# Kernel tuning notes

Hardware: AMD Instinct MI355X
Metric: run time of the kernel (lower is better)

Reference implementation:

```python
import jax, jax.numpy as jnp
import numpy as np

OMEGA = 30.0

def _conv1x1(x, W, b):
    # x: [B, Cin, D, H, W]; W: [Cout, Cin]; b: [Cout]
    return jnp.einsum('oi,bidhw->bodhw', W, x) + b[None, :, None, None, None]

def setup_inputs() -> dict:
    key = jax.random.key(0)
    ks = jax.random.split(key, 12)
    B, D, H, Wd = 1, 8, 128, 128
    C = 256
    shp = (B, 3, D, H, Wd)
    std = np.sqrt(6.0 / C) / OMEGA
    return {
        'z': jax.random.normal(ks[0], shp, jnp.float32),
        'n': jax.random.normal(ks[1], shp, jnp.float32),
        'ad': jax.random.normal(ks[2], shp, jnp.float32),
        's': jax.random.normal(ks[3], shp, jnp.float32),
        'pixel_coords': jax.random.uniform(ks[4], shp, jnp.float32),
        'view_direction': jax.random.normal(ks[5], shp, jnp.float32),
        'W1': jax.random.normal(ks[6], (C, 12), jnp.float32) * std,
        'b1': jax.random.normal(ks[7], (C,), jnp.float32) * std,
        'W2': jax.random.normal(ks[8], (C, C), jnp.float32) * std,
        'b2': jax.random.normal(ks[9], (C,), jnp.float32) * std,
        'W4': jax.random.normal(ks[10], (3, C), jnp.float32) * 1e-4,
        'b4': jax.random.normal(ks[11], (3,), jnp.float32) * 1e-4,
    }

def reference(z, n, ad, s, pixel_coords, view_direction, W1, b1, W2, b2, W4, b4):
    # concat along channel dim: [B, 12, D, H, W]
    x = jnp.concatenate((s, n, pixel_coords, view_direction), axis=1)
    h = jnp.sin(OMEGA * _conv1x1(x, W1, b1))
    h = jnp.sin(OMEGA * _conv1x1(h, W2, b2))
    s_out = 0.5 * jnp.sin(OMEGA * _conv1x1(h, W4, b4))
    # lighting_predict_mode == 'total'
    return z + s_out
```

## Files before the change

### kernel.cpp

```cpp
#include <hip/hip_runtime.h>
#include <hip/hip_bf16.h>

#define NPIX (8*128*128)
#define CH   256

typedef __attribute__((ext_vector_type(8))) short bf16x8;
typedef __attribute__((ext_vector_type(4))) float f32x4;

__device__ inline unsigned int pkbf(float a, float b) {
    union { __hip_bfloat162 h; unsigned int u; } c;
    c.h = __float22bfloat162_rn(float2{a, b});
    return c.u;
}
__device__ inline unsigned short f2bf(float f) {
    unsigned int u = __float_as_uint(f);
    return (unsigned short)((u + 0x7FFFu + ((u >> 16) & 1u)) >> 16);
}

__global__ __launch_bounds__(256) void conv_weights(
    const float* __restrict__ W1, const float* __restrict__ W2,
    const float* __restrict__ W4,
    unsigned short* __restrict__ W2b, unsigned short* __restrict__ W1b,
    unsigned short* __restrict__ W4b)
{
    if (blockIdx.x < 256) {
        const int i = blockIdx.x * 256 + threadIdx.x;
        W2b[i] = f2bf(W2[i]);
    } else {
        const int t = threadIdx.x;
        #pragma unroll
        for (int j = 0; j < 16; ++j)
            W1b[t*16 + j] = (j < 12) ? f2bf(W1[t*12 + j]) : (unsigned short)0;
        #pragma unroll
        for (int r = 0; r < 16; ++r)
            W4b[r*CH + t] = (r < 3) ? f2bf(W4[r*CH + t]) : (unsigned short)0;
    }
}

template<bool PRE>
__global__ __launch_bounds__(256, 3) void rendernet_fused2(
    const float* __restrict__ z,
    const float* __restrict__ nrm,
    const float* __restrict__ sph,
    const float* __restrict__ pc,
    const float* __restrict__ vd,
    const float* __restrict__ W1,
    const float* __restrict__ b1,
    const float* __restrict__ W2f,
    const unsigned short* __restrict__ W2b,
    const unsigned short* __restrict__ W1b,
    const float* __restrict__ b2,
    const float* __restrict__ W4f,
    const unsigned short* __restrict__ W4b,
    const float* __restrict__ b4,
    float* __restrict__ out)
{
    __shared__ __align__(16) char smem[64*512 + 64*80];
    char* xb = smem + 64*512;

    const int tid     = threadIdx.x;
    const int lane    = tid & 63;
    const int wave    = tid >> 6;
    const int lm      = lane & 15;
    const int lg      = lane >> 4;
    const int n0      = wave * 64;
    const int pixbase = blockIdx.x * 64;

    if constexpr (PRE) {
        {
            const int gp = pixbase + lane;
            union { unsigned int w[4]; bf16x8 v; } t;
            t.w[0] = t.w[1] = t.w[2] = t.w[3] = 0u;
            if (wave == 0) {
                t.w[0] = pkbf(sph[0*NPIX+gp], sph[1*NPIX+gp]);
                t.w[1] = pkbf(sph[2*NPIX+gp], nrm[0*NPIX+gp]);
                t.w[2] = pkbf(nrm[1*NPIX+gp], nrm[2*NPIX+gp]);
                t.w[3] = pkbf(pc [0*NPIX+gp], pc [1*NPIX+gp]);
            } else if (wave == 1) {
                t.w[0] = pkbf(pc[2*NPIX+gp], vd[0*NPIX+gp]);
                t.w[1] = pkbf(vd[1*NPIX+gp], vd[2*NPIX+gp]);
            }
            *(bf16x8*)(xb + lane*80 + wave*16) = t.v;
        }
        __syncthreads();

        f32x4 a1c[4][4];
        #pragma unroll
        for (int i = 0; i < 4; ++i)
            #pragma unroll
            for (int j = 0; j < 4; ++j) a1c[i][j] = (f32x4){0.f,0.f,0.f,0.f};

        bf16x8 w1frag[4];
        #pragma unroll
        for (int nf = 0; nf < 4; ++nf) {
            const int row = n0 + nf*16 + lm;
            bf16x8 t = *(const bf16x8*)(W1b + row*16 + (lg & 1)*8);
            w1frag[nf] = (lg < 2) ? t : (bf16x8){0,0,0,0,0,0,0,0};
        }
        bf16x8 ax[4];
        #pragma unroll
        for (int mf = 0; mf < 4; ++mf)
            ax[mf] = *(const bf16x8*)(xb + (mf*16 + lm)*80 + lg*16);

        #pragma unroll
        for (int nf = 0; nf < 4; ++nf)
            #pragma unroll
            for (int mf = 0; mf < 4; ++mf)
                a1c[mf][nf] = __builtin_amdgcn_mfma_f32_16x16x32_bf16(
                                  ax[mf], w1frag[nf], a1c[mf][nf], 0, 0, 0);

        float b1v[4];
        #pragma unroll
        for (int nf = 0; nf < 4; ++nf) b1v[nf] = b1[n0 + nf*16 + lm];

        #pragma unroll
        for (int mf = 0; mf < 4; ++mf)
            #pragma unroll
            for (int nf = 0; nf < 4; ++nf)
                #pragma unroll
                for (int r = 0; r < 4; ++r) {
                    const int pix = mf*16 + lg*4 + r;
                    const int ch  = n0 + nf*16 + lm;
                    *(unsigned short*)(smem + pix*512 + ((ch*2) ^ ((pix & 31) << 4))) =
                        f2bf(__sinf(30.0f * (a1c[mf][nf][r] + b1v[nf])));
                }
    } else {
        const int gp  = pixbase + lane;
        const int swz = (lane & 31) << 4;
        float xv[12];
        #pragma unroll
        for (int k = 0; k < 3; ++k) xv[k]     = sph[k*NPIX + gp];
        #pragma unroll
        for (int k = 0; k < 3; ++k) xv[3 + k] = nrm[k*NPIX + gp];
        #pragma unroll
        for (int k = 0; k < 3; ++k) xv[6 + k] = pc [k*NPIX + gp];
        #pragma unroll
        for (int k = 0; k < 3; ++k) xv[9 + k] = vd [k*NPIX + gp];
        #pragma unroll
        for (int cc = 0; cc < 64; cc += 8) {
            float hv[8];
            #pragma unroll
            for (int u = 0; u < 8; ++u) {
                const int c = n0 + cc + u;
                float a = b1[c];
                #pragma unroll
                for (int k = 0; k < 12; ++k) a += W1[c*12 + k] * xv[k];
                hv[u] = __sinf(30.0f * a);
            }
            union { unsigned int w[4]; bf16x8 v; } tp;
            #pragma unroll
            for (int u = 0; u < 4; ++u) tp.w[u] = pkbf(hv[2*u], hv[2*u+1]);
            *(bf16x8*)(smem + lane*512 + (((n0 + cc)*2) ^ swz)) = tp.v;
        }
    }
    __syncthreads();

    float b2v[4];
    #pragma unroll
    for (int nf = 0; nf < 4; ++nf) b2v[nf] = b2[n0 + nf*16 + lm];

    f32x4 acc[4][4];
    #pragma unroll
    for (int i = 0; i < 4; ++i)
        #pragma unroll
        for (int j = 0; j < 4; ++j) acc[i][j] = (f32x4){0.f,0.f,0.f,0.f};

    if constexpr (PRE) {
        const unsigned short* bp = W2b + (n0 + lm)*CH + lg*8;
        #pragma unroll
        for (int k0i = 0; k0i < 8; ++k0i) {
            bf16x8 bfr[4];
            #pragma unroll
            for (int nf = 0; nf < 4; ++nf)
                bfr[nf] = *(const bf16x8*)(bp + nf*16*CH + k0i*32);
            bf16x8 afr[4];
            #pragma unroll
            for (int mf = 0; mf < 4; ++mf) {
                const int pr = mf*16 + lm;
                afr[mf] = *(const bf16x8*)(smem + pr*512 +
                              (((k0i*32 + lg*8)*2) ^ ((pr & 31) << 4)));
            }
            #pragma unroll
            for (int nf = 0; nf < 4; ++nf)
                #pragma unroll
                for (int mf = 0; mf < 4; ++mf)
                    acc[mf][nf] = __builtin_amdgcn_mfma_f32_16x16x32_bf16(
                                      afr[mf], bfr[nf], acc[mf][nf], 0, 0, 0);
        }
    } else {
        const float* wp = W2f + (n0 + lm)*CH + lg*8;
        #pragma unroll
        for (int k0i = 0; k0i < 8; ++k0i) {
            bf16x8 afr[4];
            #pragma unroll
            for (int mf = 0; mf < 4; ++mf) {
                const int pr = mf*16 + lm;
                afr[mf] = *(const bf16x8*)(smem + pr*512 +
                              (((k0i*32 + lg*8)*2) ^ ((pr & 31) << 4)));
            }
            #pragma unroll
            for (int nf = 0; nf < 4; ++nf) {
                f32x4 lo = *(const f32x4*)(wp + nf*16*CH + k0i*32);
                f32x4 hi = *(const f32x4*)(wp + nf*16*CH + k0i*32 + 4);
                union { unsigned int w[4]; bf16x8 v; } t;
                t.w[0] = pkbf(lo[0], lo[1]);  t.w[1] = pkbf(lo[2], lo[3]);
                t.w[2] = pkbf(hi[0], hi[1]);  t.w[3] = pkbf(hi[2], hi[3]);
                #pragma unroll
                for (int mf = 0; mf < 4; ++mf)
                    acc[mf][nf] = __builtin_amdgcn_mfma_f32_16x16x32_bf16(
                                      afr[mf], t.v, acc[mf][nf], 0, 0, 0);
            }
        }
    }
    __syncthreads();

    #pragma unroll
    for (int mf = 0; mf < 4; ++mf)
        #pragma unroll
        for (int nf = 0; nf < 4; ++nf)
            #pragma unroll
            for (int r = 0; r < 4; ++r) {
                const int pix = mf*16 + lg*4 + r;
                const int ch  = n0 + nf*16 + lm;
                *(unsigned short*)(smem + pix*512 + ((ch*2) ^ ((pix & 31) << 4))) =
                    f2bf(__sinf(30.0f * (acc[mf][nf][r] + b2v[nf])));
            }
    __syncthreads();

    if (wave == 0) {
        bf16x8 w4r[8];
        if constexpr (PRE) {
            const unsigned short* bp = W4b + lm*CH + lg*8;
            #pragma unroll
            for (int k0i = 0; k0i < 8; ++k0i)
                w4r[k0i] = *(const bf16x8*)(bp + k0i*32);
        } else {
            const int c3 = (lm < 3) ? lm : 2;
            const float* fp = W4f + c3*CH + lg*8;
            #pragma unroll
            for (int k0i = 0; k0i < 8; ++k0i) {
                f32x4 lo = *(const f32x4*)(fp + k0i*32);
                f32x4 hi = *(const f32x4*)(fp + k0i*32 + 4);
                union { unsigned int w[4]; bf16x8 v; } tc;
                tc.w[0] = pkbf(lo[0], lo[1]);  tc.w[1] = pkbf(lo[2], lo[3]);
                tc.w[2] = pkbf(hi[0], hi[1]);  tc.w[3] = pkbf(hi[2], hi[3]);
                w4r[k0i] = tc.v;
            }
        }

        f32x4 d[4];
        #pragma unroll
        for (int i = 0; i < 4; ++i) d[i] = (f32x4){0.f,0.f,0.f,0.f};

        #pragma unroll
        for (int k0i = 0; k0i < 8; ++k0i) {
            bf16x8 afr[4];
            #pragma unroll
            for (int mf = 0; mf < 4; ++mf) {
                const int pr = mf*16 + lm;
                afr[mf] = *(const bf16x8*)(smem + pr*512 +
                              (((k0i*32 + lg*8)*2) ^ ((pr & 31) << 4)));
            }
            #pragma unroll
            for (int mf = 0; mf < 4; ++mf)
                d[mf] = __builtin_amdgcn_mfma_f32_16x16x32_bf16(
                            afr[mf], w4r[k0i], d[mf], 0, 0, 0);
        }

        if (lm < 3) {
            const float b4v = b4[lm];
            #pragma unroll
            for (int mf = 0; mf < 4; ++mf)
                #pragma unroll
                for (int r = 0; r < 4; ++r) {
                    const int pix = mf*16 + lg*4 + r;
                    const int gi  = lm*NPIX + pixbase + pix;
                    out[gi] = z[gi] + 0.5f * __sinf(30.0f * (d[mf][r] + b4v));
                }
        }
    }
}

extern "C" void kernel_launch(void* const* d_in, const int* in_sizes, int n_in,
                              void* d_out, int out_size, void* d_ws, size_t ws_size,
                              hipStream_t stream) {
    const float* z   = (const float*)d_in[0];
    const float* nrm = (const float*)d_in[1];
    const float* s   = (const float*)d_in[3];
    const float* pc  = (const float*)d_in[4];
    const float* vd  = (const float*)d_in[5];
    const float* W1  = (const float*)d_in[6];
    const float* b1  = (const float*)d_in[7];
    const float* W2  = (const float*)d_in[8];
    const float* b2  = (const float*)d_in[9];
    const float* W4  = (const float*)d_in[10];
    const float* b4  = (const float*)d_in[11];
    float* out = (float*)d_out;

    const size_t need = (size_t)(CH*CH + 16*CH + 16*CH) * sizeof(unsigned short);
    if (ws_size >= need) {
        unsigned short* W2b = (unsigned short*)d_ws;
        unsigned short* W1b = W2b + CH*CH;
        unsigned short* W4b = W1b + 16*CH;
        conv_weights<<<dim3(257), dim3(256), 0, stream>>>(W1, W2, W4, W2b, W1b, W4b);
        rendernet_fused2<true><<<dim3(NPIX/64), dim3(256), 0, stream>>>(
            z, nrm, s, pc, vd, W1, b1, W2, W2b, W1b, b2, W4, W4b, b4, out);
    } else {
        rendernet_fused2<false><<<dim3(NPIX/64), dim3(256), 0, stream>>>(
            z, nrm, s, pc, vd, W1, b1, W2, nullptr, nullptr, b2, W4, nullptr, b4, out);
    }
}
```

Before: 143.4 us.

## Split channels across eight waves with permuted K layout and packed stores

Raises the block to 512 threads (8 waves), so each wave covers 32 output channels instead of 64. This halves per-wave accumulator registers and aims for more waves per CU. The K dimension of W2 and W4 is permuted at conversion time so each lane can write two adjacent channels as one packed 32-bit store to LDS instead of scalar 16-bit stores. Biases are folded into the accumulator initialisation. In exchange the weight fragment reuse per wave drops and W2 is read by twice as many waves per block.

```diff
diff --git a/kernel.cpp b/kernel.cpp
--- a/kernel.cpp
+++ b/kernel.cpp
@@ -15,6 +15,9 @@
 __device__ inline unsigned short f2bf(float f) {
     unsigned int u = __float_as_uint(f);
     return (unsigned short)((u + 0x7FFFu + ((u >> 16) & 1u)) >> 16);
+}
+__device__ inline int kperm32(int k) {
+    return (k & ~31) | ((k & 15) << 1) | ((k >> 4) & 1);
 }
 
 __global__ __launch_bounds__(256) void conv_weights(
@@ -24,21 +27,22 @@
     unsigned short* __restrict__ W4b)
 {
     if (blockIdx.x < 256) {
-        const int i = blockIdx.x * 256 + threadIdx.x;
-        W2b[i] = f2bf(W2[i]);
+        const int o = blockIdx.x, k = threadIdx.x;
+        W2b[o*CH + kperm32(k)] = f2bf(W2[o*CH + k]);
     } else {
         const int t = threadIdx.x;
         #pragma unroll
         for (int j = 0; j < 16; ++j)
             W1b[t*16 + j] = (j < 12) ? f2bf(W1[t*12 + j]) : (unsigned short)0;
+        const int kp = kperm32(t);
         #pragma unroll
         for (int r = 0; r < 16; ++r)
-            W4b[r*CH + t] = (r < 3) ? f2bf(W4[r*CH + t]) : (unsigned short)0;
+            W4b[r*CH + kp] = (r < 3) ? f2bf(W4[r*CH + t]) : (unsigned short)0;
     }
 }
 
 template<bool PRE>
-__global__ __launch_bounds__(256, 3) void rendernet_fused2(
+__global__ __launch_bounds__(512, 4) void rendernet3(
     const float* __restrict__ z,
     const float* __restrict__ nrm,
     const float* __restrict__ sph,
@@ -63,39 +67,42 @@
     const int wave    = tid >> 6;
     const int lm      = lane & 15;
     const int lg      = lane >> 4;
-    const int n0      = wave * 64;
+    const int n0      = wave * 32;
     const int pixbase = blockIdx.x * 64;
+
+    f32x4 acc[4][2];
 
     if constexpr (PRE) {
         {
             const int gp = pixbase + lane;
-            union { unsigned int w[4]; bf16x8 v; } t;
-            t.w[0] = t.w[1] = t.w[2] = t.w[3] = 0u;
+            unsigned int w0 = 0u, w1 = 0u;
             if (wave == 0) {
-                t.w[0] = pkbf(sph[0*NPIX+gp], sph[1*NPIX+gp]);
-                t.w[1] = pkbf(sph[2*NPIX+gp], nrm[0*NPIX+gp]);
-                t.w[2] = pkbf(nrm[1*NPIX+gp], nrm[2*NPIX+gp]);
-                t.w[3] = pkbf(pc [0*NPIX+gp], pc [1*NPIX+gp]);
+                w0 = pkbf(sph[0*NPIX+gp], sph[1*NPIX+gp]);
+                w1 = pkbf(sph[2*NPIX+gp], nrm[0*NPIX+gp]);
             } else if (wave == 1) {
-                t.w[0] = pkbf(pc[2*NPIX+gp], vd[0*NPIX+gp]);
-                t.w[1] = pkbf(vd[1*NPIX+gp], vd[2*NPIX+gp]);
-            }
-            *(bf16x8*)(xb + lane*80 + wave*16) = t.v;
+                w0 = pkbf(nrm[1*NPIX+gp], nrm[2*NPIX+gp]);
+                w1 = pkbf(pc [0*NPIX+gp], pc [1*NPIX+gp]);
+            } else if (wave == 2) {
+                w0 = pkbf(pc[2*NPIX+gp], vd[0*NPIX+gp]);
+                w1 = pkbf(vd[1*NPIX+gp], vd[2*NPIX+gp]);
+            }
+            *(unsigned int*)(xb + lane*80 + wave*8)     = w0;
+            *(unsigned int*)(xb + lane*80 + wave*8 + 4) = w1;
         }
         __syncthreads();
 
-        f32x4 a1c[4][4];
-        #pragma unroll
-        for (int i = 0; i < 4; ++i)
-            #pragma unroll
-            for (int j = 0; j < 4; ++j) a1c[i][j] = (f32x4){0.f,0.f,0.f,0.f};
-
-        bf16x8 w1frag[4];
-        #pragma unroll
-        for (int nf = 0; nf < 4; ++nf) {
-            const int row = n0 + nf*16 + lm;
-            bf16x8 t = *(const bf16x8*)(W1b + row*16 + (lg & 1)*8);
-            w1frag[nf] = (lg < 2) ? t : (bf16x8){0,0,0,0,0,0,0,0};
+        #pragma unroll
+        for (int nf = 0; nf < 2; ++nf) {
+            const float bv = b1[n0 + nf*16 + lm];
+            #pragma unroll
+            for (int mf = 0; mf < 4; ++mf) acc[mf][nf] = (f32x4){bv, bv, bv, bv};
+        }
+
+        bf16x8 w1f[2];
+        #pragma unroll
+        for (int nf = 0; nf < 2; ++nf) {
+            bf16x8 t = *(const bf16x8*)(W1b + (n0 + nf*16 + lm)*16 + (lg & 1)*8);
+            w1f[nf] = (lg < 2) ? t : (bf16x8){0,0,0,0,0,0,0,0};
         }
         bf16x8 ax[4];
         #pragma unroll
@@ -103,30 +110,23 @@
             ax[mf] = *(const bf16x8*)(xb + (mf*16 + lm)*80 + lg*16);
 
         #pragma unroll
-        for (int nf = 0; nf < 4; ++nf)
+        for (int nf = 0; nf < 2; ++nf)
             #pragma unroll
             for (int mf = 0; mf < 4; ++mf)
-                a1c[mf][nf] = __builtin_amdgcn_mfma_f32_16x16x32_bf16(
-                                  ax[mf], w1frag[nf], a1c[mf][nf], 0, 0, 0);
-
-        float b1v[4];
-        #pragma unroll
-        for (int nf = 0; nf < 4; ++nf) b1v[nf] = b1[n0 + nf*16 + lm];
+                acc[mf][nf] = __builtin_amdgcn_mfma_f32_16x16x32_bf16(
+                                  ax[mf], w1f[nf], acc[mf][nf], 0, 0, 0);
 
         #pragma unroll
         for (int mf = 0; mf < 4; ++mf)
             #pragma unroll
-            for (int nf = 0; nf < 4; ++nf)
-                #pragma unroll
-                for (int r = 0; r < 4; ++r) {
-                    const int pix = mf*16 + lg*4 + r;
-                    const int ch  = n0 + nf*16 + lm;
-                    *(unsigned short*)(smem + pix*512 + ((ch*2) ^ ((pix & 31) << 4))) =
-                        f2bf(__sinf(30.0f * (a1c[mf][nf][r] + b1v[nf])));
-                }
-    } else {
-        const int gp  = pixbase + lane;
-        const int swz = (lane & 31) << 4;
+            for (int r = 0; r < 4; ++r) {
+                const int pix = mf*16 + lg*4 + r;
+                const unsigned int pk = pkbf(__sinf(30.0f*acc[mf][0][r]),
+                                             __sinf(30.0f*acc[mf][1][r]));
+                *(unsigned int*)(smem + pix*512 + ((n0*2 + lm*4) ^ ((pix & 31) << 4))) = pk;
+            }
+    } else {
+        const int gp = pixbase + lane;
         float xv[12];
         #pragma unroll
         for (int k = 0; k < 3; ++k) xv[k]     = sph[k*NPIX + gp];
@@ -137,58 +137,48 @@
         #pragma unroll
         for (int k = 0; k < 3; ++k) xv[9 + k] = vd [k*NPIX + gp];
         #pragma unroll
-        for (int cc = 0; cc < 64; cc += 8) {
-            float hv[8];
-            #pragma unroll
-            for (int u = 0; u < 8; ++u) {
-                const int c = n0 + cc + u;
-                float a = b1[c];
-                #pragma unroll
-                for (int k = 0; k < 12; ++k) a += W1[c*12 + k] * xv[k];
-                hv[u] = __sinf(30.0f * a);
-            }
-            union { unsigned int w[4]; bf16x8 v; } tp;
-            #pragma unroll
-            for (int u = 0; u < 4; ++u) tp.w[u] = pkbf(hv[2*u], hv[2*u+1]);
-            *(bf16x8*)(smem + lane*512 + (((n0 + cc)*2) ^ swz)) = tp.v;
+        for (int c = 0; c < 32; ++c) {
+            const int cc = n0 + c;
+            float a = b1[cc];
+            #pragma unroll
+            for (int k = 0; k < 12; ++k) a += W1[cc*12 + k] * xv[k];
+            const int kp = n0 + ((c & 15) << 1) + (c >> 4);
+            *(unsigned short*)(smem + lane*512 + ((kp*2) ^ ((lane & 31) << 4))) =
+                f2bf(__sinf(30.0f * a));
         }
     }
     __syncthreads();
 
-    float b2v[4];
     #pragma unroll
-    for (int nf = 0; nf < 4; ++nf) b2v[nf] = b2[n0 + nf*16 + lm];
-
-    f32x4 acc[4][4];
-    #pragma unroll
-    for (int i = 0; i < 4; ++i)
-        #pragma unroll
-        for (int j = 0; j < 4; ++j) acc[i][j] = (f32x4){0.f,0.f,0.f,0.f};
+    for (int nf = 0; nf < 2; ++nf) {
+        const float bv = b2[n0 + nf*16 + lm];
+        #pragma unroll
+        for (int mf = 0; mf < 4; ++mf) acc[mf][nf] = (f32x4){bv, bv, bv, bv};
+    }
 
     if constexpr (PRE) {
         const unsigned short* bp = W2b + (n0 + lm)*CH + lg*8;
         #pragma unroll
         for (int k0i = 0; k0i < 8; ++k0i) {
-            bf16x8 bfr[4];
-            #pragma unroll
-            for (int nf = 0; nf < 4; ++nf)
+            bf16x8 bfr[2];
+            #pragma unroll
+            for (int nf = 0; nf < 2; ++nf)
                 bfr[nf] = *(const bf16x8*)(bp + nf*16*CH + k0i*32);
             bf16x8 afr[4];
             #pragma unroll
             for (int mf = 0; mf < 4; ++mf) {
                 const int pr = mf*16 + lm;
                 afr[mf] = *(const bf16x8*)(smem + pr*512 +
-                              (((k0i*32 + lg*8)*2) ^ ((pr & 31) << 4)));
-            }
-            #pragma unroll
-            for (int nf = 0; nf < 4; ++nf)
+                              ((k0i*64 + lg*16) ^ ((pr & 31) << 4)));
+            }
+            #pragma unroll
+            for (int nf = 0; nf < 2; ++nf)
                 #pragma unroll
                 for (int mf = 0; mf < 4; ++mf)
                     acc[mf][nf] = __builtin_amdgcn_mfma_f32_16x16x32_bf16(
                                       afr[mf], bfr[nf], acc[mf][nf], 0, 0, 0);
         }
     } else {
-        const float* wp = W2f + (n0 + lm)*CH + lg*8;
         #pragma unroll
         for (int k0i = 0; k0i < 8; ++k0i) {
             bf16x8 afr[4];
@@ -196,19 +186,21 @@
             for (int mf = 0; mf < 4; ++mf) {
                 const int pr = mf*16 + lm;
                 afr[mf] = *(const bf16x8*)(smem + pr*512 +
-                              (((k0i*32 + lg*8)*2) ^ ((pr & 31) << 4)));
-            }
-            #pragma unroll
-            for (int nf = 0; nf < 4; ++nf) {
-                f32x4 lo = *(const f32x4*)(wp + nf*16*CH + k0i*32);
-                f32x4 hi = *(const f32x4*)(wp + nf*16*CH + k0i*32 + 4);
-                union { unsigned int w[4]; bf16x8 v; } t;
-                t.w[0] = pkbf(lo[0], lo[1]);  t.w[1] = pkbf(lo[2], lo[3]);
-                t.w[2] = pkbf(hi[0], hi[1]);  t.w[3] = pkbf(hi[2], hi[3]);
+                              ((k0i*64 + lg*16) ^ ((pr & 31) << 4)));
+            }
+            #pragma unroll
+            for (int nf = 0; nf < 2; ++nf) {
+                bf16x8 t;
+                #pragma unroll
+                for (int j = 0; j < 8; ++j) {
+                    const int kp = k0i*32 + lg*8 + j;
+                    const int kr = (kp & ~31) | ((kp & 1) << 4) | ((kp >> 1) & 15);
+                    t[j] = (short)f2bf(W2f[(n0 + nf*16 + lm)*CH + kr]);
+                }
                 #pragma unroll
                 for (int mf = 0; mf < 4; ++mf)
                     acc[mf][nf] = __builtin_amdgcn_mfma_f32_16x16x32_bf16(
-                                      afr[mf], t.v, acc[mf][nf], 0, 0, 0);
+                                      afr[mf], t, acc[mf][nf], 0, 0, 0);
             }
         }
     }
@@ -217,65 +209,54 @@
     #pragma unroll
     for (int mf = 0; mf < 4; ++mf)
         #pragma unroll
-        for (int nf = 0; nf < 4; ++nf)
-            #pragma unroll
-            for (int r = 0; r < 4; ++r) {
-                const int pix = mf*16 + lg*4 + r;
-                const int ch  = n0 + nf*16 + lm;
-                *(unsigned short*)(smem + pix*512 + ((ch*2) ^ ((pix & 31) << 4))) =
-                    f2bf(__sinf(30.0f * (acc[mf][nf][r] + b2v[nf])));
-            }
+        for (int r = 0; r < 4; ++r) {
+            const int pix = mf*16 + lg*4 + r;
+            const unsigned int pk = pkbf(__sinf(30.0f*acc[mf][0][r]),
+                                         __sinf(30.0f*acc[mf][1][r]));
+            *(unsigned int*)(smem + pix*512 + ((n0*2 + lm*4) ^ ((pix & 31) << 4))) = pk;
+        }
     __syncthreads();
 
     if (wave == 0) {
-        bf16x8 w4r[8];
-        if constexpr (PRE) {
-            const unsigned short* bp = W4b + lm*CH + lg*8;
-            #pragma unroll
-            for (int k0i = 0; k0i < 8; ++k0i)
-                w4r[k0i] = *(const bf16x8*)(bp + k0i*32);
-        } else {
-            const int c3 = (lm < 3) ? lm : 2;
-            const float* fp = W4f + c3*CH + lg*8;
-            #pragma unroll
-            for (int k0i = 0; k0i < 8; ++k0i) {
-                f32x4 lo = *(const f32x4*)(fp + k0i*32);
-                f32x4 hi = *(const f32x4*)(fp + k0i*32 + 4);
-                union { unsigned int w[4]; bf16x8 v; } tc;
-                tc.w[0] = pkbf(lo[0], lo[1]);  tc.w[1] = pkbf(lo[2], lo[3]);
-                tc.w[2] = pkbf(hi[0], hi[1]);  tc.w[3] = pkbf(hi[2], hi[3]);
-                w4r[k0i] = tc.v;
-            }
-        }
-
+        const float b4v = (lm < 3) ? b4[lm] : 0.0f;
         f32x4 d[4];
         #pragma unroll
-        for (int i = 0; i < 4; ++i) d[i] = (f32x4){0.f,0.f,0.f,0.f};
+        for (int mf = 0; mf < 4; ++mf) d[mf] = (f32x4){b4v, b4v, b4v, b4v};
 
         #pragma unroll
         for (int k0i = 0; k0i < 8; ++k0i) {
+            bf16x8 b4f;
+            if constexpr (PRE) {
+                b4f = *(const bf16x8*)(W4b + lm*CH + k0i*32 + lg*8);
+            } else {
+                #pragma unroll
+                for (int j = 0; j < 8; ++j) {
+                    const int kp = k0i*32 + lg*8 + j;
+                    const int kr = (kp & ~31) | ((kp & 1) << 4) | ((kp >> 1) & 15);
+                    b4f[j] = (lm < 3) ? (short)f2bf(W4f[lm*CH + kr]) : (short)0;
+                }
+            }
             bf16x8 afr[4];
             #pragma unroll
             for (int mf = 0; mf < 4; ++mf) {
                 const int pr = mf*16 + lm;
                 afr[mf] = *(const bf16x8*)(smem + pr*512 +
-                              (((k0i*32 + lg*8)*2) ^ ((pr & 31) << 4)));
+                              ((k0i*64 + lg*16) ^ ((pr & 31) << 4)));
             }
             #pragma unroll
             for (int mf = 0; mf < 4; ++mf)
                 d[mf] = __builtin_amdgcn_mfma_f32_16x16x32_bf16(
-                            afr[mf], w4r[k0i], d[mf], 0, 0, 0);
+                            afr[mf], b4f, d[mf], 0, 0, 0);
         }
 
         if (lm < 3) {
-            const float b4v = b4[lm];
             #pragma unroll
             for (int mf = 0; mf < 4; ++mf)
                 #pragma unroll
                 for (int r = 0; r < 4; ++r) {
                     const int pix = mf*16 + lg*4 + r;
                     const int gi  = lm*NPIX + pixbase + pix;
-                    out[gi] = z[gi] + 0.5f * __sinf(30.0f * (d[mf][r] + b4v));
+                    out[gi] = z[gi] + 0.5f * __sinf(30.0f * d[mf][r]);
                 }
         }
     }
@@ -303,10 +284,10 @@
         unsigned short* W1b = W2b + CH*CH;
         unsigned short* W4b = W1b + 16*CH;
         conv_weights<<<dim3(257), dim3(256), 0, stream>>>(W1, W2, W4, W2b, W1b, W4b);
-        rendernet_fused2<true><<<dim3(NPIX/64), dim3(256), 0, stream>>>(
+        rendernet3<true><<<dim3(NPIX/64), dim3(512), 0, stream>>>(
             z, nrm, s, pc, vd, W1, b1, W2, W2b, W1b, b2, W4, W4b, b4, out);
     } else {
-        rendernet_fused2<false><<<dim3(NPIX/64), dim3(256), 0, stream>>>(
+        rendernet3<false><<<dim3(NPIX/64), dim3(512), 0, stream>>>(
             z, nrm, s, pc, vd, W1, b1, W2, nullptr, nullptr, b2, W4, nullptr, b4, out);
     }
 }
```

After: 125.3 us. 12.7% less time.
